# Kernel tuning notes

Measured on AMD Instinct MI355X. Metric: run time of the kernel, lower is better.

The kernel has to match this reference:

```python
import jax, jax.numpy as jnp
import numpy as np

N_GRAPHS = 500  # number of graphs in the batched DGLGraph


def _lin_init(key, fan_in, fan_out):
    k1, k2 = jax.random.split(key)
    s = 1.0 / np.sqrt(fan_in)
    W = jax.random.uniform(k1, (fan_in, fan_out), jnp.float32, -s, s)
    b = jax.random.uniform(k2, (fan_out,), jnp.float32, -s, s)
    return W, b


def setup_inputs() -> dict:
    key = jax.random.key(0)
    ks = jax.random.split(key, 12)
    N, E, F_IN, H, F_OUT = 50000, 600000, 74, 128, 1
    x = jax.random.normal(ks[0], (N, F_IN), jnp.float32)
    src = jax.random.randint(ks[1], (E,), 0, N)
    dst = jax.random.randint(ks[2], (E,), 0, N)
    graph_ids = jnp.sort(jax.random.randint(ks[3], (N,), 0, N_GRAPHS))
    W_in, b_in = _lin_init(ks[4], F_IN, H)
    W_g0, b_g0 = _lin_init(ks[5], H, H)
    W_g1, b_g1 = _lin_init(ks[6], H, H)
    W_g2, b_g2 = _lin_init(ks[7], H, H)
    W_out, b_out = _lin_init(ks[8], H, H)
    W_ff, b_ff = _lin_init(ks[9], H, F_OUT)
    return dict(x=x, W_in=W_in, b_in=b_in, W_g0=W_g0, b_g0=b_g0,
                W_g1=W_g1, b_g1=b_g1, W_g2=W_g2, b_g2=b_g2,
                W_out=W_out, b_out=b_out, W_ff=W_ff, b_ff=b_ff,
                src=src, dst=dst, graph_ids=graph_ids)


def reference(x, W_in, b_in, W_g0, b_g0, W_g1, b_g1, W_g2, b_g2,
              W_out, b_out, W_ff, b_ff, src, dst, graph_ids):
    N = x.shape[0]
    # DGL GraphConv norm='both', allow_zero_in_degree=True -> clamp degrees at 1
    ones = jnp.ones(src.shape, x.dtype)
    out_deg = jnp.zeros((N,), x.dtype).at[src].add(ones)
    in_deg = jnp.zeros((N,), x.dtype).at[dst].add(ones)
    out_norm = jnp.maximum(out_deg, 1.0) ** -0.5  # [N]
    in_norm = jnp.maximum(in_deg, 1.0) ** -0.5    # [N]

    def gconv(h, W, b):
        m = (h * out_norm[:, None])[src]            # gather: [E, H]
        agg = jnp.zeros_like(h).at[dst].add(m)      # scatter-sum: [N, H]
        return (agg * in_norm[:, None]) @ W + b

    h = jax.nn.silu(x @ W_in + b_in)                # embedding_in
    for W, b in ((W_g0, b_g0), (W_g1, b_g1), (W_g2, b_g2)):
        h = jax.nn.silu(gconv(h, W, b))             # GraphConv + activation
    h = h @ W_out + b_out                           # embedding_out
    pooled = jax.ops.segment_sum(h, graph_ids, num_segments=N_GRAPHS)  # sum_nodes
    return pooled @ W_ff + b_ff                     # ff -> [N_GRAPHS, 1]
```

## Files before the change

### kernel.cpp

```cpp
#include <hip/hip_runtime.h>
#include <math.h>

#define H 128
#define RBITS 13
#define RSIZE 8192
#define NCHUNK 96

typedef __attribute__((ext_vector_type(8))) short bf16x8;
typedef __attribute__((ext_vector_type(4))) float f32x4;

__device__ inline unsigned short f2bf(float f) {
  unsigned u = __float_as_uint(f);
  return (unsigned short)((u + 0x7FFF + ((u >> 16) & 1)) >> 16);
}

__global__ __launch_bounds__(256) void k_hist(const int* __restrict__ src,
                                              const int* __restrict__ dst,
                                              int* __restrict__ ppack, int E) {
  int r = blockIdx.x / NCHUNK, c = blockIdx.x % NCHUNK;
  int base = r << RBITS;
  __shared__ int h[RSIZE];
  for (int i = threadIdx.x; i < RSIZE; i += 256) h[i] = 0;
  __syncthreads();
  int e0 = (int)(((long long)E * c) / NCHUNK);
  int e1 = (int)(((long long)E * (c + 1)) / NCHUNK);
  for (int e = e0 + threadIdx.x; e < e1; e += 256) {
    unsigned ls = (unsigned)(src[e] - base);
    if (ls < RSIZE) atomicAdd(&h[ls], 1);
    unsigned ld = (unsigned)(dst[e] - base);
    if (ld < RSIZE) atomicAdd(&h[ld], 0x10000);
  }
  __syncthreads();
  int* p = ppack + (((size_t)(r * NCHUNK + c)) << RBITS);
  for (int i = threadIdx.x; i < RSIZE; i += 256) p[i] = h[i];
}

__global__ void k_reduce(int* __restrict__ ppack,
                         int* __restrict__ ind, float* __restrict__ onorm,
                         float* __restrict__ inorm, int N) {
  int i = blockIdx.x * blockDim.x + threadIdx.x;
  if (i >= N) return;
  int r = i >> RBITS, l = i & (RSIZE - 1);
  size_t rb = ((size_t)r * NCHUNK) << RBITS;
  int sumS = 0, run = 0;
  for (int c = 0; c < NCHUNK; ++c) {
    size_t idx = rb + ((size_t)c << RBITS) + l;
    int v = ppack[idx];
    sumS += v & 0xFFFF;
    ppack[idx] = run;
    run += (v >> 16) & 0xFFFF;
  }
  ind[i] = run;
  int od = sumS < 1 ? 1 : sumS;
  int id = run < 1 ? 1 : run;
  onorm[i] = rsqrtf((float)od);
  inorm[i] = rsqrtf((float)id);
}

__global__ __launch_bounds__(1024) void k_scan_blocks(const int* __restrict__ counts,
                                                      int* __restrict__ row_ptr,
                                                      int* __restrict__ blk_sums, int N) {
  __shared__ int buf[1024];
  int i = blockIdx.x * 1024 + threadIdx.x;
  int v = (i < N) ? counts[i] : 0;
  buf[threadIdx.x] = v;
  __syncthreads();
#pragma unroll
  for (int off = 1; off < 1024; off <<= 1) {
    int t = 0;
    if (threadIdx.x >= off) t = buf[threadIdx.x - off];
    __syncthreads();
    if (threadIdx.x >= off) buf[threadIdx.x] += t;
    __syncthreads();
  }
  if (i < N) row_ptr[i] = buf[threadIdx.x] - v;
  if (threadIdx.x == 1023) blk_sums[blockIdx.x] = buf[1023];
}

__global__ __launch_bounds__(1024) void k_scan_tops(int* __restrict__ blk_sums,
                                                    int* __restrict__ blk_offs,
                                                    int* __restrict__ row_ptr,
                                                    int nb, int N) {
  __shared__ int buf[1024];
  int v = (threadIdx.x < nb) ? blk_sums[threadIdx.x] : 0;
  buf[threadIdx.x] = v;
  __syncthreads();
#pragma unroll
  for (int off = 1; off < 1024; off <<= 1) {
    int t = 0;
    if (threadIdx.x >= off) t = buf[threadIdx.x - off];
    __syncthreads();
    if (threadIdx.x >= off) buf[threadIdx.x] += t;
    __syncthreads();
  }
  if (threadIdx.x < nb) blk_offs[threadIdx.x] = buf[threadIdx.x] - v;
  if (threadIdx.x == 1023) row_ptr[N] = buf[1023];
}

__global__ void k_scan_add(int* __restrict__ row_ptr, const int* __restrict__ blk_offs, int N) {
  int i = blockIdx.x * blockDim.x + threadIdx.x;
  if (i < N) row_ptr[i] += blk_offs[i >> 10];
}

__global__ __launch_bounds__(256) void k_fill_nr(const int* __restrict__ src,
                                                 const int* __restrict__ dst,
                                                 const int* __restrict__ row_ptr,
                                                 const int* __restrict__ ppfx,
                                                 int* __restrict__ csr, int N, int E) {
  int r = blockIdx.x / NCHUNK, c = blockIdx.x % NCHUNK;
  int base = r << RBITS;
  __shared__ int cur[RSIZE];
  const int* pd = ppfx + (((size_t)(r * NCHUNK + c)) << RBITS);
  for (int i = threadIdx.x; i < RSIZE; i += 256) {
    int node = base + i;
    cur[i] = (node < N) ? (row_ptr[node] + pd[i]) : 0;
  }
  __syncthreads();
  int e0 = (int)(((long long)E * c) / NCHUNK);
  int e1 = (int)(((long long)E * (c + 1)) / NCHUNK);
  for (int e = e0 + threadIdx.x; e < e1; e += 256) {
    unsigned ld = (unsigned)(dst[e] - base);
    if (ld < RSIZE) {
      int pos = atomicAdd(&cur[ld], 1);
      csr[pos] = src[e];
    }
  }
}

struct WSplitArgs {
  const float* W[5];
  int K[5];
  int off[6];
};
__global__ __launch_bounds__(256) void k_wsplit(WSplitArgs a, short* __restrict__ hi_buf,
                                                short* __restrict__ lo_buf) {
  int idx = blockIdx.x * 256 + threadIdx.x;
  if (idx >= a.off[5]) return;
  int wsel = 0;
  while (idx >= a.off[wsel + 1]) ++wsel;
  int lidx = idx - a.off[wsel];
  int j  = lidx & 7;
  int ln = (lidx >> 3) & 63;
  int ct = (lidx >> 9) & 7;
  int kt = lidx >> 12;
  int k = (kt << 5) | ((ln >> 4) << 3) | j;
  int n = (ct << 4) | (ln & 15);
  float v = (k < a.K[wsel]) ? a.W[wsel][(size_t)k * H + n] : 0.f;
  unsigned short hi = f2bf(v);
  float hif = __uint_as_float((unsigned)hi << 16);
  unsigned short lo = f2bf(v - hif);
  hi_buf[idx] = (short)hi;
  lo_buf[idx] = (short)lo;
}

__global__ __launch_bounds__(256) void k_gemm_mfma(const float* __restrict__ A,
                                                   const short* __restrict__ whi,
                                                   const short* __restrict__ wlo,
                                                   const float* __restrict__ bias,
                                                   const float* __restrict__ onorm,
                                                   float* __restrict__ out_f,
                                                   unsigned short* __restrict__ out_bf,
                                                   int N, int K, int do_silu) {
  const int t = threadIdx.x;
  const int w = t >> 6;
  const int l = t & 63;
  const int q = l >> 4;
  const int m = l & 15;
  const int rbase = blockIdx.x * 64 + w * 16;
  const int row = rbase + m;
  const bool rowOK = row < N;
  const float* Ap = A + (size_t)(rowOK ? row : 0) * K;
  const int KT = (K + 31) >> 5;

  f32x4 acc[8];
#pragma unroll
  for (int ct = 0; ct < 8; ++ct) acc[ct] = (f32x4){0.f, 0.f, 0.f, 0.f};

  for (int kt = 0; kt < KT; ++kt) {
    int kbase = kt * 32 + q * 8;
    float f[8];
    if (rowOK && kbase + 8 <= K) {
      float4 f0 = *(const float4*)(Ap + kbase);
      float4 f1 = *(const float4*)(Ap + kbase + 4);
      f[0] = f0.x; f[1] = f0.y; f[2] = f0.z; f[3] = f0.w;
      f[4] = f1.x; f[5] = f1.y; f[6] = f1.z; f[7] = f1.w;
    } else {
#pragma unroll
      for (int j = 0; j < 8; ++j)
        f[j] = (rowOK && kbase + j < K) ? Ap[kbase + j] : 0.f;
    }
    union { bf16x8 v; short s[8]; } ah, al;
#pragma unroll
    for (int j = 0; j < 8; ++j) {
      unsigned short hi = f2bf(f[j]);
      ah.s[j] = (short)hi;
      float hif = __uint_as_float((unsigned)hi << 16);
      al.s[j] = (short)f2bf(f[j] - hif);
    }
    const short* bh_base = whi + ((size_t)(kt * 8) * 64 + l) * 8;
    const short* bl_base = wlo + ((size_t)(kt * 8) * 64 + l) * 8;
#pragma unroll
    for (int ct = 0; ct < 8; ++ct) {
      bf16x8 bh = *(const bf16x8*)(bh_base + (size_t)ct * 512);
      bf16x8 bl = *(const bf16x8*)(bl_base + (size_t)ct * 512);
      acc[ct] = __builtin_amdgcn_mfma_f32_16x16x32_bf16(ah.v, bh, acc[ct], 0, 0, 0);
      acc[ct] = __builtin_amdgcn_mfma_f32_16x16x32_bf16(al.v, bh, acc[ct], 0, 0, 0);
      acc[ct] = __builtin_amdgcn_mfma_f32_16x16x32_bf16(ah.v, bl, acc[ct], 0, 0, 0);
    }
  }

  int orow[4]; bool ok[4]; float on_[4];
#pragma unroll
  for (int r = 0; r < 4; ++r) {
    orow[r] = rbase + q * 4 + r;
    ok[r] = orow[r] < N;
    on_[r] = (out_bf && ok[r]) ? onorm[orow[r]] : 0.f;
  }
#pragma unroll
  for (int ct = 0; ct < 8; ++ct) {
    int col = ct * 16 + m;
    float bcol = bias[col];
    if (out_bf) {
#pragma unroll
      for (int r = 0; r < 4; ++r) {
        if (ok[r]) {
          float v = acc[ct][r] + bcol;
          v = v / (1.f + expf(-v));
          out_bf[(size_t)orow[r] * H + col] = f2bf(v * on_[r]);
        }
      }
    } else {
#pragma unroll
      for (int r = 0; r < 4; ++r) {
        if (ok[r]) {
          float v = acc[ct][r] + bcol;
          if (do_silu) v = v / (1.f + expf(-v));
          out_f[(size_t)orow[r] * H + col] = v;
        }
      }
    }
  }
}

__global__ __launch_bounds__(256) void k_final(const float* __restrict__ A,
                                               const short* __restrict__ whi2,
                                               const short* __restrict__ wlo2,
                                               const float* __restrict__ b2,
                                               const short* __restrict__ whio,
                                               const short* __restrict__ wloo,
                                               const float* __restrict__ bo,
                                               const int* __restrict__ gid,
                                               float* __restrict__ pooled, int N) {
  __shared__ float As[64][132];
  const int t = threadIdx.x;
  const int w = t >> 6, l = t & 63, q = l >> 4, m = l & 15;
  const int blk0 = blockIdx.x * 64;
  const int rbase = blk0 + w * 16;
  const int row = rbase + m;
  const bool rowOK = row < N;
  const float* Ap = A + (size_t)(rowOK ? row : 0) * H;

  f32x4 acc[8];
#pragma unroll
  for (int ct = 0; ct < 8; ++ct) acc[ct] = (f32x4){0.f, 0.f, 0.f, 0.f};

#pragma unroll
  for (int kt = 0; kt < 4; ++kt) {
    int kbase = kt * 32 + q * 8;
    float f[8];
    if (rowOK) {
      float4 f0 = *(const float4*)(Ap + kbase);
      float4 f1 = *(const float4*)(Ap + kbase + 4);
      f[0] = f0.x; f[1] = f0.y; f[2] = f0.z; f[3] = f0.w;
      f[4] = f1.x; f[5] = f1.y; f[6] = f1.z; f[7] = f1.w;
    } else {
#pragma unroll
      for (int j = 0; j < 8; ++j) f[j] = 0.f;
    }
    union { bf16x8 v; short s[8]; } ah, al;
#pragma unroll
    for (int j = 0; j < 8; ++j) {
      unsigned short hi = f2bf(f[j]);
      ah.s[j] = (short)hi;
      float hif = __uint_as_float((unsigned)hi << 16);
      al.s[j] = (short)f2bf(f[j] - hif);
    }
    const short* bh_base = whi2 + ((size_t)(kt * 8) * 64 + l) * 8;
    const short* bl_base = wlo2 + ((size_t)(kt * 8) * 64 + l) * 8;
#pragma unroll
    for (int ct = 0; ct < 8; ++ct) {
      bf16x8 bh = *(const bf16x8*)(bh_base + (size_t)ct * 512);
      bf16x8 bl = *(const bf16x8*)(bl_base + (size_t)ct * 512);
      acc[ct] = __builtin_amdgcn_mfma_f32_16x16x32_bf16(ah.v, bh, acc[ct], 0, 0, 0);
      acc[ct] = __builtin_amdgcn_mfma_f32_16x16x32_bf16(al.v, bh, acc[ct], 0, 0, 0);
      acc[ct] = __builtin_amdgcn_mfma_f32_16x16x32_bf16(ah.v, bl, acc[ct], 0, 0, 0);
    }
  }
#pragma unroll
  for (int ct = 0; ct < 8; ++ct) {
    int col = ct * 16 + m;
    float bcol = b2[col];
#pragma unroll
    for (int r = 0; r < 4; ++r) {
      float v = acc[ct][r] + bcol;
      v = v / (1.f + expf(-v));
      As[w * 16 + q * 4 + r][col] = v;
    }
  }
  __syncthreads();

#pragma unroll
  for (int ct = 0; ct < 8; ++ct) acc[ct] = (f32x4){0.f, 0.f, 0.f, 0.f};
#pragma unroll
  for (int kt = 0; kt < 4; ++kt) {
    int kbase = kt * 32 + q * 8;
    float f[8];
    *(float4*)&f[0] = *(const float4*)(&As[w * 16 + m][kbase]);
    *(float4*)&f[4] = *(const float4*)(&As[w * 16 + m][kbase + 4]);
    union { bf16x8 v; short s[8]; } ah, al;
#pragma unroll
    for (int j = 0; j < 8; ++j) {
      unsigned short hi = f2bf(f[j]);
      ah.s[j] = (short)hi;
      float hif = __uint_as_float((unsigned)hi << 16);
      al.s[j] = (short)f2bf(f[j] - hif);
    }
    const short* bh_base = whio + ((size_t)(kt * 8) * 64 + l) * 8;
    const short* bl_base = wloo + ((size_t)(kt * 8) * 64 + l) * 8;
#pragma unroll
    for (int ct = 0; ct < 8; ++ct) {
      bf16x8 bh = *(const bf16x8*)(bh_base + (size_t)ct * 512);
      bf16x8 bl = *(const bf16x8*)(bl_base + (size_t)ct * 512);
      acc[ct] = __builtin_amdgcn_mfma_f32_16x16x32_bf16(ah.v, bh, acc[ct], 0, 0, 0);
      acc[ct] = __builtin_amdgcn_mfma_f32_16x16x32_bf16(al.v, bh, acc[ct], 0, 0, 0);
      acc[ct] = __builtin_amdgcn_mfma_f32_16x16x32_bf16(ah.v, bl, acc[ct], 0, 0, 0);
    }
  }
  __syncthreads();
#pragma unroll
  for (int ct = 0; ct < 8; ++ct) {
    int col = ct * 16 + m;
    float bcol = bo[col];
#pragma unroll
    for (int r = 0; r < 4; ++r)
      As[w * 16 + q * 4 + r][col] = acc[ct][r] + bcol;
  }
  __syncthreads();

  if (t < H) {
    int vend = N - blk0; if (vend > 64) vend = 64;
    if (vend > 0) {
      int cur = gid[blk0];
      float s = 0.f;
      for (int i = 0; i < vend; ++i) {
        int g = gid[blk0 + i];
        if (g != cur) {
          atomicAdd(&pooled[(size_t)cur * H + t], s);
          s = 0.f; cur = g;
        }
        s += As[i][t];
      }
      atomicAdd(&pooled[(size_t)cur * H + t], s);
    }
  }
}

__global__ __launch_bounds__(64) void k_gather_bf(const unsigned* __restrict__ hb,
                                                  const int* __restrict__ csr_src,
                                                  const int* __restrict__ row_ptr,
                                                  const float* __restrict__ inorm,
                                                  float* __restrict__ agg, int N) {
  int v = blockIdx.x;
  int t = threadIdx.x;
  int b = row_ptr[v], e = row_ptr[v + 1];
  float ax = 0.f, ay = 0.f;
  for (int i = b; i < e; ++i) {
    int s = csr_src[i];
    unsigned p = hb[(size_t)s * 64 + t];
    ax += __uint_as_float(p << 16);
    ay += __uint_as_float(p & 0xFFFF0000u);
  }
  float inn = inorm[v];
  *(float2*)(agg + (size_t)v * H + t * 2) = make_float2(ax * inn, ay * inn);
}

__global__ __launch_bounds__(128) void k_ff(const float* __restrict__ pooled,
                                            const float* __restrict__ Wff,
                                            const float* __restrict__ bff,
                                            float* __restrict__ out, int G) {
  int g = blockIdx.x;
  int t = threadIdx.x;
  float v = pooled[(size_t)g * H + t] * Wff[t];
#pragma unroll
  for (int off = 32; off > 0; off >>= 1) v += __shfl_down(v, off, 64);
  __shared__ float red[2];
  if ((t & 63) == 0) red[t >> 6] = v;
  __syncthreads();
  if (t == 0) out[g] = red[0] + red[1] + bff[0];
}

extern "C" void kernel_launch(void* const* d_in, const int* in_sizes, int n_in,
                              void* d_out, int out_size, void* d_ws, size_t ws_size,
                              hipStream_t stream) {
  const float* x     = (const float*)d_in[0];
  const float* W_in  = (const float*)d_in[1];
  const float* b_in  = (const float*)d_in[2];
  const float* W_g0  = (const float*)d_in[3];
  const float* b_g0  = (const float*)d_in[4];
  const float* W_g1  = (const float*)d_in[5];
  const float* b_g1  = (const float*)d_in[6];
  const float* W_g2  = (const float*)d_in[7];
  const float* b_g2  = (const float*)d_in[8];
  const float* W_out = (const float*)d_in[9];
  const float* b_out = (const float*)d_in[10];
  const float* W_ff  = (const float*)d_in[11];
  const float* b_ff  = (const float*)d_in[12];
  const int* src = (const int*)d_in[13];
  const int* dst = (const int*)d_in[14];
  const int* gid = (const int*)d_in[15];
  float* out = (float*)d_out;

  const int N = in_sizes[15];
  const int E = in_sizes[13];
  const int K_IN = in_sizes[1] / H;
  const int G = out_size;

  char* ws = (char*)d_ws;
  size_t off = 0;
  auto alloc = [&](size_t bytes) -> void* {
    void* p = ws + off;
    off = (off + bytes + 255) & ~(size_t)255;
    return p;
  };
  float*          agg  = (float*)alloc((size_t)N * H * 4);
  unsigned short* hb0  = (unsigned short*)alloc((size_t)N * H * 2);
  unsigned short* hb1  = (unsigned short*)alloc((size_t)N * H * 2);
  float* onorm   = (float*)alloc((size_t)N * 4);
  float* inorm   = (float*)alloc((size_t)N * 4);
  int*   ind     = (int*)alloc((size_t)N * 4);
  int*   row_ptr = (int*)alloc((size_t)(N + 1) * 4);
  int*   csr     = (int*)alloc((size_t)E * 4);
  float* pooled  = (float*)alloc((size_t)G * H * 4);
  int nb = (N + 1023) / 1024;
  int*   blk_sums = (int*)alloc((size_t)nb * 4);
  int*   blk_offs = (int*)alloc((size_t)nb * 4);

  const int KT_IN = (K_IN + 31) >> 5;
  const int fr_in = KT_IN * 4096, fr_h = 4 * 4096;
  const int total_fr = fr_in + 4 * fr_h;
  short* whi_buf = (short*)alloc((size_t)total_fr * 2);
  short* wlo_buf = (short*)alloc((size_t)total_fr * 2);

  int nr = (N + RSIZE - 1) / RSIZE;
  int* ppack = (int*)agg;

  hipMemsetAsync(pooled, 0, (size_t)G * H * 4, stream);

  WSplitArgs wa;
  wa.W[0] = W_in;  wa.W[1] = W_g0; wa.W[2] = W_g1; wa.W[3] = W_g2; wa.W[4] = W_out;
  wa.K[0] = K_IN;  wa.K[1] = H;    wa.K[2] = H;    wa.K[3] = H;    wa.K[4] = H;
  wa.off[0] = 0;
  wa.off[1] = fr_in;
  for (int i = 2; i <= 5; ++i) wa.off[i] = wa.off[i - 1] + fr_h;
  k_wsplit<<<(total_fr + 255) / 256, 256, 0, stream>>>(wa, whi_buf, wlo_buf);

  k_hist<<<nr * NCHUNK, 256, 0, stream>>>(src, dst, ppack, E);
  k_reduce<<<(N + 255) / 256, 256, 0, stream>>>(ppack, ind, onorm, inorm, N);
  k_scan_blocks<<<nb, 1024, 0, stream>>>(ind, row_ptr, blk_sums, N);
  k_scan_tops<<<1, 1024, 0, stream>>>(blk_sums, blk_offs, row_ptr, nb, N);
  k_scan_add<<<(N + 255) / 256, 256, 0, stream>>>(row_ptr, blk_offs, N);
  k_fill_nr<<<nr * NCHUNK, 256, 0, stream>>>(src, dst, row_ptr, ppack, csr, N, E);

  int gblk = (N + 63) / 64;
  short* whi_in = whi_buf + wa.off[0]; short* wlo_in = wlo_buf + wa.off[0];
  short* whi_g0 = whi_buf + wa.off[1]; short* wlo_g0 = wlo_buf + wa.off[1];
  short* whi_g1 = whi_buf + wa.off[2]; short* wlo_g1 = wlo_buf + wa.off[2];
  short* whi_g2 = whi_buf + wa.off[3]; short* wlo_g2 = wlo_buf + wa.off[3];
  short* whi_o  = whi_buf + wa.off[4]; short* wlo_o  = wlo_buf + wa.off[4];

  k_gemm_mfma<<<gblk, 256, 0, stream>>>(x, whi_in, wlo_in, b_in, onorm, nullptr, hb0, N, K_IN, 1);

  k_gather_bf<<<N, 64, 0, stream>>>((const unsigned*)hb0, csr, row_ptr, inorm, agg, N);
  k_gemm_mfma<<<gblk, 256, 0, stream>>>(agg, whi_g0, wlo_g0, b_g0, onorm, nullptr, hb1, N, H, 1);
  k_gather_bf<<<N, 64, 0, stream>>>((const unsigned*)hb1, csr, row_ptr, inorm, agg, N);
  k_gemm_mfma<<<gblk, 256, 0, stream>>>(agg, whi_g1, wlo_g1, b_g1, onorm, nullptr, hb0, N, H, 1);
  k_gather_bf<<<N, 64, 0, stream>>>((const unsigned*)hb0, csr, row_ptr, inorm, agg, N);
  k_final<<<gblk, 256, 0, stream>>>(agg, whi_g2, wlo_g2, b_g2, whi_o, wlo_o, b_out,
                                    gid, pooled, N);

  k_ff<<<G, 128, 0, stream>>>(pooled, W_ff, b_ff, out, G);
}
```

Baseline: 365.8 us.

## Fuse graph preprocessing and input GEMM into fewer kernel launches

Merges the pooled zeroing, the input embedding GEMM and the degree histogram into one k_front launch. Degree reduction and the row-pointer scan collapse into a single k_mid kernel that uses an atomic global counter in place of a three-kernel scan. Because the input GEMM now runs before the norms exist, the out-degree norm is applied inside the first gather. This cuts several launches and lets the GEMM overlap the histogram, at the cost of a non-deterministic CSR row ordering across blocks and extra indirect onorm loads in the first gather.

Measured after the change: 359.7 us. About the same (-1.7%).

```diff
diff --git a/kernel.cpp b/kernel.cpp
--- a/kernel.cpp
+++ b/kernel.cpp
@@ -12,119 +12,6 @@
 __device__ inline unsigned short f2bf(float f) {
   unsigned u = __float_as_uint(f);
   return (unsigned short)((u + 0x7FFF + ((u >> 16) & 1)) >> 16);
-}
-
-__global__ __launch_bounds__(256) void k_hist(const int* __restrict__ src,
-                                              const int* __restrict__ dst,
-                                              int* __restrict__ ppack, int E) {
-  int r = blockIdx.x / NCHUNK, c = blockIdx.x % NCHUNK;
-  int base = r << RBITS;
-  __shared__ int h[RSIZE];
-  for (int i = threadIdx.x; i < RSIZE; i += 256) h[i] = 0;
-  __syncthreads();
-  int e0 = (int)(((long long)E * c) / NCHUNK);
-  int e1 = (int)(((long long)E * (c + 1)) / NCHUNK);
-  for (int e = e0 + threadIdx.x; e < e1; e += 256) {
-    unsigned ls = (unsigned)(src[e] - base);
-    if (ls < RSIZE) atomicAdd(&h[ls], 1);
-    unsigned ld = (unsigned)(dst[e] - base);
-    if (ld < RSIZE) atomicAdd(&h[ld], 0x10000);
-  }
-  __syncthreads();
-  int* p = ppack + (((size_t)(r * NCHUNK + c)) << RBITS);
-  for (int i = threadIdx.x; i < RSIZE; i += 256) p[i] = h[i];
-}
-
-__global__ void k_reduce(int* __restrict__ ppack,
-                         int* __restrict__ ind, float* __restrict__ onorm,
-                         float* __restrict__ inorm, int N) {
-  int i = blockIdx.x * blockDim.x + threadIdx.x;
-  if (i >= N) return;
-  int r = i >> RBITS, l = i & (RSIZE - 1);
-  size_t rb = ((size_t)r * NCHUNK) << RBITS;
-  int sumS = 0, run = 0;
-  for (int c = 0; c < NCHUNK; ++c) {
-    size_t idx = rb + ((size_t)c << RBITS) + l;
-    int v = ppack[idx];
-    sumS += v & 0xFFFF;
-    ppack[idx] = run;
-    run += (v >> 16) & 0xFFFF;
-  }
-  ind[i] = run;
-  int od = sumS < 1 ? 1 : sumS;
-  int id = run < 1 ? 1 : run;
-  onorm[i] = rsqrtf((float)od);
-  inorm[i] = rsqrtf((float)id);
-}
-
-__global__ __launch_bounds__(1024) void k_scan_blocks(const int* __restrict__ counts,
-                                                      int* __restrict__ row_ptr,
-                                                      int* __restrict__ blk_sums, int N) {
-  __shared__ int buf[1024];
-  int i = blockIdx.x * 1024 + threadIdx.x;
-  int v = (i < N) ? counts[i] : 0;
-  buf[threadIdx.x] = v;
-  __syncthreads();
-#pragma unroll
-  for (int off = 1; off < 1024; off <<= 1) {
-    int t = 0;
-    if (threadIdx.x >= off) t = buf[threadIdx.x - off];
-    __syncthreads();
-    if (threadIdx.x >= off) buf[threadIdx.x] += t;
-    __syncthreads();
-  }
-  if (i < N) row_ptr[i] = buf[threadIdx.x] - v;
-  if (threadIdx.x == 1023) blk_sums[blockIdx.x] = buf[1023];
-}
-
-__global__ __launch_bounds__(1024) void k_scan_tops(int* __restrict__ blk_sums,
-                                                    int* __restrict__ blk_offs,
-                                                    int* __restrict__ row_ptr,
-                                                    int nb, int N) {
-  __shared__ int buf[1024];
-  int v = (threadIdx.x < nb) ? blk_sums[threadIdx.x] : 0;
-  buf[threadIdx.x] = v;
-  __syncthreads();
-#pragma unroll
-  for (int off = 1; off < 1024; off <<= 1) {
-    int t = 0;
-    if (threadIdx.x >= off) t = buf[threadIdx.x - off];
-    __syncthreads();
-    if (threadIdx.x >= off) buf[threadIdx.x] += t;
-    __syncthreads();
-  }
-  if (threadIdx.x < nb) blk_offs[threadIdx.x] = buf[threadIdx.x] - v;
-  if (threadIdx.x == 1023) row_ptr[N] = buf[1023];
-}
-
-__global__ void k_scan_add(int* __restrict__ row_ptr, const int* __restrict__ blk_offs, int N) {
-  int i = blockIdx.x * blockDim.x + threadIdx.x;
-  if (i < N) row_ptr[i] += blk_offs[i >> 10];
-}
-
-__global__ __launch_bounds__(256) void k_fill_nr(const int* __restrict__ src,
-                                                 const int* __restrict__ dst,
-                                                 const int* __restrict__ row_ptr,
-                                                 const int* __restrict__ ppfx,
-                                                 int* __restrict__ csr, int N, int E) {
-  int r = blockIdx.x / NCHUNK, c = blockIdx.x % NCHUNK;
-  int base = r << RBITS;
-  __shared__ int cur[RSIZE];
-  const int* pd = ppfx + (((size_t)(r * NCHUNK + c)) << RBITS);
-  for (int i = threadIdx.x; i < RSIZE; i += 256) {
-    int node = base + i;
-    cur[i] = (node < N) ? (row_ptr[node] + pd[i]) : 0;
-  }
-  __syncthreads();
-  int e0 = (int)(((long long)E * c) / NCHUNK);
-  int e1 = (int)(((long long)E * (c + 1)) / NCHUNK);
-  for (int e = e0 + threadIdx.x; e < e1; e += 256) {
-    unsigned ld = (unsigned)(dst[e] - base);
-    if (ld < RSIZE) {
-      int pos = atomicAdd(&cur[ld], 1);
-      csr[pos] = src[e];
-    }
-  }
 }
 
 struct WSplitArgs {
@@ -153,20 +40,20 @@
   lo_buf[idx] = (short)lo;
 }
 
-__global__ __launch_bounds__(256) void k_gemm_mfma(const float* __restrict__ A,
-                                                   const short* __restrict__ whi,
-                                                   const short* __restrict__ wlo,
-                                                   const float* __restrict__ bias,
-                                                   const float* __restrict__ onorm,
-                                                   float* __restrict__ out_f,
-                                                   unsigned short* __restrict__ out_bf,
-                                                   int N, int K, int do_silu) {
-  const int t = threadIdx.x;
-  const int w = t >> 6;
-  const int l = t & 63;
+__device__ __forceinline__ void gemm_body(int blk, int tid,
+                                          const float* __restrict__ A,
+                                          const short* __restrict__ whi,
+                                          const short* __restrict__ wlo,
+                                          const float* __restrict__ bias,
+                                          const float* __restrict__ onorm,
+                                          float* __restrict__ out_f,
+                                          unsigned short* __restrict__ out_bf,
+                                          int N, int K, int do_silu) {
+  const int w = tid >> 6;
+  const int l = tid & 63;
   const int q = l >> 4;
   const int m = l & 15;
-  const int rbase = blockIdx.x * 64 + w * 16;
+  const int rbase = blk * 64 + w * 16;
   const int row = rbase + m;
   const bool rowOK = row < N;
   const float* Ap = A + (size_t)(rowOK ? row : 0) * K;
@@ -214,7 +101,7 @@
   for (int r = 0; r < 4; ++r) {
     orow[r] = rbase + q * 4 + r;
     ok[r] = orow[r] < N;
-    on_[r] = (out_bf && ok[r]) ? onorm[orow[r]] : 0.f;
+    on_[r] = (out_bf && onorm && ok[r]) ? onorm[orow[r]] : 1.f;
   }
 #pragma unroll
   for (int ct = 0; ct < 8; ++ct) {
@@ -240,6 +127,158 @@
       }
     }
   }
+}
+
+__global__ __launch_bounds__(256) void k_gemm_mfma(const float* __restrict__ A,
+                                                   const short* __restrict__ whi,
+                                                   const short* __restrict__ wlo,
+                                                   const float* __restrict__ bias,
+                                                   const float* __restrict__ onorm,
+                                                   float* __restrict__ out_f,
+                                                   unsigned short* __restrict__ out_bf,
+                                                   int N, int K, int do_silu) {
+  gemm_body(blockIdx.x, threadIdx.x, A, whi, wlo, bias, onorm, out_f, out_bf, N, K, do_silu);
+}
+
+__global__ __launch_bounds__(256) void k_front(const int* __restrict__ src,
+                                               const int* __restrict__ dst,
+                                               int* __restrict__ ppack, int E,
+                                               const float* __restrict__ x,
+                                               const short* __restrict__ whi_in,
+                                               const short* __restrict__ wlo_in,
+                                               const float* __restrict__ b_in,
+                                               unsigned short* __restrict__ hb0,
+                                               float* __restrict__ pooled, int GH,
+                                               int* __restrict__ gcount,
+                                               int N, int K_IN, int zb, int gblk) {
+  __shared__ int h[RSIZE];
+  int b = blockIdx.x;
+  int t = threadIdx.x;
+  if (b < zb) {
+    int idx = b * 256 + t;
+    if (idx < GH) pooled[idx] = 0.f;
+    if (b == 0 && t == 0) *gcount = 0;
+    return;
+  }
+  b -= zb;
+  if (b < gblk) {
+    gemm_body(b, t, x, whi_in, wlo_in, b_in, nullptr, nullptr, hb0, N, K_IN, 1);
+    return;
+  }
+  b -= gblk;
+  int r = b / NCHUNK, c = b % NCHUNK;
+  int base = r << RBITS;
+  for (int i = t; i < RSIZE; i += 256) h[i] = 0;
+  __syncthreads();
+  int e0 = (int)(((long long)E * c) / NCHUNK);
+  int e1 = (int)(((long long)E * (c + 1)) / NCHUNK);
+  for (int e = e0 + t; e < e1; e += 256) {
+    unsigned ls = (unsigned)(src[e] - base);
+    if (ls < RSIZE) atomicAdd(&h[ls], 1);
+    unsigned ld = (unsigned)(dst[e] - base);
+    if (ld < RSIZE) atomicAdd(&h[ld], 0x10000);
+  }
+  __syncthreads();
+  int* p = ppack + (((size_t)(r * NCHUNK + c)) << RBITS);
+  for (int i = t; i < RSIZE; i += 256) p[i] = h[i];
+}
+
+__global__ __launch_bounds__(1024) void k_mid(int* __restrict__ ppack,
+                                              int* __restrict__ deg,
+                                              float* __restrict__ onorm,
+                                              float* __restrict__ inorm,
+                                              int* __restrict__ row_start,
+                                              int* __restrict__ gcount, int N) {
+  __shared__ int buf[1024];
+  __shared__ int base_s;
+  int i = blockIdx.x * 1024 + threadIdx.x;
+  int run = 0;
+  if (i < N) {
+    int r = i >> RBITS, l = i & (RSIZE - 1);
+    size_t rb = ((size_t)r * NCHUNK) << RBITS;
+    int sumS = 0;
+    for (int c = 0; c < NCHUNK; ++c) {
+      size_t idx = rb + ((size_t)c << RBITS) + l;
+      int v = ppack[idx];
+      sumS += v & 0xFFFF;
+      ppack[idx] = run;
+      run += (v >> 16) & 0xFFFF;
+    }
+    deg[i] = run;
+    int od = sumS < 1 ? 1 : sumS;
+    int id = run < 1 ? 1 : run;
+    onorm[i] = rsqrtf((float)od);
+    inorm[i] = rsqrtf((float)id);
+  }
+  buf[threadIdx.x] = run;
+  __syncthreads();
+#pragma unroll
+  for (int off = 1; off < 1024; off <<= 1) {
+    int tv = 0;
+    if (threadIdx.x >= off) tv = buf[threadIdx.x - off];
+    __syncthreads();
+    if (threadIdx.x >= off) buf[threadIdx.x] += tv;
+    __syncthreads();
+  }
+  if (threadIdx.x == 1023) base_s = atomicAdd(gcount, buf[1023]);
+  __syncthreads();
+  if (i < N) row_start[i] = base_s + buf[threadIdx.x] - run;
+}
+
+__global__ __launch_bounds__(256) void k_fill_nr(const int* __restrict__ src,
+                                                 const int* __restrict__ dst,
+                                                 const int* __restrict__ row_start,
+                                                 const int* __restrict__ ppfx,
+                                                 int* __restrict__ csr, int N, int E) {
+  int r = blockIdx.x / NCHUNK, c = blockIdx.x % NCHUNK;
+  int base = r << RBITS;
+  __shared__ int cur[RSIZE];
+  const int* pd = ppfx + (((size_t)(r * NCHUNK + c)) << RBITS);
+  for (int i = threadIdx.x; i < RSIZE; i += 256) {
+    int node = base + i;
+    cur[i] = (node < N) ? (row_start[node] + pd[i]) : 0;
+  }
+  __syncthreads();
+  int e0 = (int)(((long long)E * c) / NCHUNK);
+  int e1 = (int)(((long long)E * (c + 1)) / NCHUNK);
+  for (int e = e0 + threadIdx.x; e < e1; e += 256) {
+    unsigned ld = (unsigned)(dst[e] - base);
+    if (ld < RSIZE) {
+      int pos = atomicAdd(&cur[ld], 1);
+      csr[pos] = src[e];
+    }
+  }
+}
+
+__global__ __launch_bounds__(64) void k_gather_bf(const unsigned* __restrict__ hb,
+                                                  const int* __restrict__ csr_src,
+                                                  const int* __restrict__ row_start,
+                                                  const int* __restrict__ deg,
+                                                  const float* __restrict__ onorm,
+                                                  const float* __restrict__ inorm,
+                                                  float* __restrict__ agg, int N) {
+  int v = blockIdx.x;
+  int t = threadIdx.x;
+  int b = row_start[v], e = b + deg[v];
+  float ax = 0.f, ay = 0.f;
+  if (onorm) {
+    for (int i = b; i < e; ++i) {
+      int s = csr_src[i];
+      float on = onorm[s];
+      unsigned p = hb[(size_t)s * 64 + t];
+      ax += __uint_as_float(p << 16) * on;
+      ay += __uint_as_float(p & 0xFFFF0000u) * on;
+    }
+  } else {
+    for (int i = b; i < e; ++i) {
+      int s = csr_src[i];
+      unsigned p = hb[(size_t)s * 64 + t];
+      ax += __uint_as_float(p << 16);
+      ay += __uint_as_float(p & 0xFFFF0000u);
+    }
+  }
+  float inn = inorm[v];
+  *(float2*)(agg + (size_t)v * H + t * 2) = make_float2(ax * inn, ay * inn);
 }
 
 __global__ __launch_bounds__(256) void k_final(const float* __restrict__ A,
@@ -363,25 +402,6 @@
       atomicAdd(&pooled[(size_t)cur * H + t], s);
     }
   }
-}
-
-__global__ __launch_bounds__(64) void k_gather_bf(const unsigned* __restrict__ hb,
-                                                  const int* __restrict__ csr_src,
-                                                  const int* __restrict__ row_ptr,
-                                                  const float* __restrict__ inorm,
-                                                  float* __restrict__ agg, int N) {
-  int v = blockIdx.x;
-  int t = threadIdx.x;
-  int b = row_ptr[v], e = row_ptr[v + 1];
-  float ax = 0.f, ay = 0.f;
-  for (int i = b; i < e; ++i) {
-    int s = csr_src[i];
-    unsigned p = hb[(size_t)s * 64 + t];
-    ax += __uint_as_float(p << 16);
-    ay += __uint_as_float(p & 0xFFFF0000u);
-  }
-  float inn = inorm[v];
-  *(float2*)(agg + (size_t)v * H + t * 2) = make_float2(ax * inn, ay * inn);
 }
 
 __global__ __launch_bounds__(128) void k_ff(const float* __restrict__ pooled,
@@ -435,15 +455,13 @@
   float*          agg  = (float*)alloc((size_t)N * H * 4);
   unsigned short* hb0  = (unsigned short*)alloc((size_t)N * H * 2);
   unsigned short* hb1  = (unsigned short*)alloc((size_t)N * H * 2);
-  float* onorm   = (float*)alloc((size_t)N * 4);
-  float* inorm   = (float*)alloc((size_t)N * 4);
-  int*   ind     = (int*)alloc((size_t)N * 4);
-  int*   row_ptr = (int*)alloc((size_t)(N + 1) * 4);
-  int*   csr     = (int*)alloc((size_t)E * 4);
-  float* pooled  = (float*)alloc((size_t)G * H * 4);
-  int nb = (N + 1023) / 1024;
-  int*   blk_sums = (int*)alloc((size_t)nb * 4);
-  int*   blk_offs = (int*)alloc((size_t)nb * 4);
+  float* onorm     = (float*)alloc((size_t)N * 4);
+  float* inorm     = (float*)alloc((size_t)N * 4);
+  int*   deg       = (int*)alloc((size_t)N * 4);
+  int*   row_start = (int*)alloc((size_t)N * 4);
+  int*   csr       = (int*)alloc((size_t)E * 4);
+  float* pooled    = (float*)alloc((size_t)G * H * 4);
+  int*   gcount    = (int*)alloc(256);
 
   const int KT_IN = (K_IN + 31) >> 5;
   const int fr_in = KT_IN * 4096, fr_h = 4 * 4096;
@@ -453,8 +471,6 @@
 
   int nr = (N + RSIZE - 1) / RSIZE;
   int* ppack = (int*)agg;
-
-  hipMemsetAsync(pooled, 0, (size_t)G * H * 4, stream);
 
   WSplitArgs wa;
   wa.W[0] = W_in;  wa.W[1] = W_g0; wa.W[2] = W_g1; wa.W[3] = W_g2; wa.W[4] = W_out;
@@ -464,27 +480,30 @@
   for (int i = 2; i <= 5; ++i) wa.off[i] = wa.off[i - 1] + fr_h;
   k_wsplit<<<(total_fr + 255) / 256, 256, 0, stream>>>(wa, whi_buf, wlo_buf);
 
-  k_hist<<<nr * NCHUNK, 256, 0, stream>>>(src, dst, ppack, E);
-  k_reduce<<<(N + 255) / 256, 256, 0, stream>>>(ppack, ind, onorm, inorm, N);
-  k_scan_blocks<<<nb, 1024, 0, stream>>>(ind, row_ptr, blk_sums, N);
-  k_scan_tops<<<1, 1024, 0, stream>>>(blk_sums, blk_offs, row_ptr, nb, N);
-  k_scan_add<<<(N + 255) / 256, 256, 0, stream>>>(row_ptr, blk_offs, N);
-  k_fill_nr<<<nr * NCHUNK, 256, 0, stream>>>(src, dst, row_ptr, ppack, csr, N, E);
-
-  int gblk = (N + 63) / 64;
   short* whi_in = whi_buf + wa.off[0]; short* wlo_in = wlo_buf + wa.off[0];
   short* whi_g0 = whi_buf + wa.off[1]; short* wlo_g0 = wlo_buf + wa.off[1];
   short* whi_g1 = whi_buf + wa.off[2]; short* wlo_g1 = wlo_buf + wa.off[2];
   short* whi_g2 = whi_buf + wa.off[3]; short* wlo_g2 = wlo_buf + wa.off[3];
   short* whi_o  = whi_buf + wa.off[4]; short* wlo_o  = wlo_buf + wa.off[4];
 
-  k_gemm_mfma<<<gblk, 256, 0, stream>>>(x, whi_in, wlo_in, b_in, onorm, nullptr, hb0, N, K_IN, 1);
-
-  k_gather_bf<<<N, 64, 0, stream>>>((const unsigned*)hb0, csr, row_ptr, inorm, agg, N);
+  int gblk = (N + 63) / 64;
+  int GH = G * H;
+  int zb = (GH + 255) / 256;
+  int histblk = nr * NCHUNK;
+  k_front<<<zb + gblk + histblk, 256, 0, stream>>>(src, dst, ppack, E,
+                                                   x, whi_in, wlo_in, b_in, hb0,
+                                                   pooled, GH, gcount, N, K_IN, zb, gblk);
+
+  int nb = (N + 1023) / 1024;
+  k_mid<<<nb, 1024, 0, stream>>>(ppack, deg, onorm, inorm, row_start, gcount, N);
+
+  k_fill_nr<<<histblk, 256, 0, stream>>>(src, dst, row_start, ppack, csr, N, E);
+
+  k_gather_bf<<<N, 64, 0, stream>>>((const unsigned*)hb0, csr, row_start, deg, onorm, inorm, agg, N);
   k_gemm_mfma<<<gblk, 256, 0, stream>>>(agg, whi_g0, wlo_g0, b_g0, onorm, nullptr, hb1, N, H, 1);
-  k_gather_bf<<<N, 64, 0, stream>>>((const unsigned*)hb1, csr, row_ptr, inorm, agg, N);
+  k_gather_bf<<<N, 64, 0, stream>>>((const unsigned*)hb1, csr, row_start, deg, nullptr, inorm, agg, N);
   k_gemm_mfma<<<gblk, 256, 0, stream>>>(agg, whi_g1, wlo_g1, b_g1, onorm, nullptr, hb0, N, H, 1);
-  k_gather_bf<<<N, 64, 0, stream>>>((const unsigned*)hb0, csr, row_ptr, inorm, agg, N);
+  k_gather_bf<<<N, 64, 0, stream>>>((const unsigned*)hb0, csr, row_start, deg, nullptr, inorm, agg, N);
   k_final<<<gblk, 256, 0, stream>>>(agg, whi_g2, wlo_g2, b_g2, whi_o, wlo_o, b_out,
                                     gid, pooled, N);
 
```
